# Optimization experiments

Hardware: AMD Instinct MI355X
Metric: run time of the kernel (lower is better)

The kernel has to match this reference:

```python
import jax, jax.numpy as jnp
import numpy as np

D_MODEL, D_QKV, N_HEADS, D_FFN = 2048, 128, 16, 8192
B, L = 2, 2048
EPS = 1e-8
ROPE_THETA = 10000.0


def _rope_cos_sin(seq_len, dim, dtype):
    # interleaved RoPE (rotary_embedding_torch default): pairs (0,1),(2,3),...
    inv_freq = ROPE_THETA ** (-jnp.arange(0, dim, 2, dtype=jnp.float32) / dim)
    ang = jnp.arange(seq_len, dtype=jnp.float32)[:, None] * inv_freq[None, :]  # [L, dim/2]
    return jnp.cos(ang).astype(dtype), jnp.sin(ang).astype(dtype)


def _apply_rope(t, cos, sin):
    # t: [b, h, l, d]; cos/sin: [l, d/2]
    t1, t2 = t[..., 0::2], t[..., 1::2]
    r1 = t1 * cos - t2 * sin
    r2 = t1 * sin + t2 * cos
    return jnp.stack([r1, r2], axis=-1).reshape(t.shape)


def setup_inputs() -> dict:
    key = jax.random.key(0)
    ks = jax.random.split(key, 5)
    d_out = D_QKV * N_HEADS * 3 + D_FFN * 2  # 22528
    return {
        "x": jax.random.normal(ks[0], (B, L, D_MODEL), dtype=jnp.float32),
        "g": jnp.ones((D_MODEL,), dtype=jnp.float32),
        "W_dense": jax.random.normal(ks[1], (d_out, D_MODEL), dtype=jnp.float32) * 0.02,
        "b_dense": jnp.zeros((d_out,), dtype=jnp.float32),
        "W_attn_out": jax.random.normal(ks[2], (D_MODEL, D_QKV * N_HEADS), dtype=jnp.float32) * 0.02,
        "W_ffn_out": jax.random.normal(ks[3], (D_MODEL, D_FFN), dtype=jnp.float32) * 0.02,
    }


def reference(x, g, W_dense, b_dense, W_attn_out, W_ffn_out):
    # RMSNorm (torch.norm variant): x / clamp(||x|| * d^-0.5, eps) * g
    norm = jnp.sqrt(jnp.sum(x * x, axis=-1, keepdims=True)) * (D_MODEL ** -0.5)
    normed = x / jnp.maximum(norm, EPS) * g

    h = jnp.einsum('bld,od->blo', normed, W_dense) + b_dense  # [B, L, 22528]
    dh = D_QKV * N_HEADS
    q, k, v, a, b_gate = jnp.split(h, [dh, 2 * dh, 3 * dh, 3 * dh + D_FFN], axis=-1)

    def to_heads(t):
        return t.reshape(B, L, N_HEADS, D_QKV).transpose(0, 2, 1, 3)  # [b,h,l,d]

    q, k, v = to_heads(q), to_heads(k), to_heads(v)
    cos, sin = _rope_cos_sin(L, D_QKV, x.dtype)
    q = _apply_rope(q, cos, sin)
    k = _apply_rope(k, cos, sin)

    scale = 1.0 / jnp.sqrt(jnp.asarray(D_QKV, dtype=x.dtype))
    scores = jnp.einsum('bhqd,bhkd->bhqk', q, k) * scale
    causal = jnp.tril(jnp.ones((L, L), dtype=bool))
    scores = jnp.where(causal, scores, jnp.asarray(-jnp.inf, dtype=scores.dtype))
    probs = jax.nn.softmax(scores, axis=-1)
    attn = jnp.einsum('bhqk,bhkd->bqhd', probs, v).reshape(B, L, dh)

    attn_out = jnp.einsum('blk,ok->blo', attn, W_attn_out)
    ffn_out = jnp.einsum('blf,of->blo', a * jax.nn.silu(b_gate), W_ffn_out)
    return x + attn_out + ffn_out
```

## Files before the change

kernel.cpp:

```cpp
#include <hip/hip_runtime.h>
#include <hip/hip_bf16.h>
#include <cmath>

typedef __bf16 bf16;
typedef __attribute__((ext_vector_type(8))) __bf16 bf16x8;
typedef __attribute__((ext_vector_type(4))) float f32x4;
typedef unsigned int u32;
typedef unsigned short u16;

#define D_MODEL 2048
#define NH 16
#define DQ 128
#define DH 2048
#define DFFN 8192
#define DOUT 22528
#define HQKV 6144
#define BATCH 2
#define SEQ 2048
#define NROWS 4096

__device__ __forceinline__ void gload16(const void* g, void* l) {
    __builtin_amdgcn_global_load_lds((__attribute__((address_space(1))) const void*)g,
                                     (__attribute__((address_space(3))) void*)l, 16, 0, 0);
}

__device__ __forceinline__ float bf2f(u16 u) {
    union { u32 i; float f; } c; c.i = ((u32)u) << 16; return c.f;
}

#define VMW(n)  asm volatile("s_waitcnt vmcnt(" #n ")" ::: "memory")
#define LGK0()  asm volatile("s_waitcnt lgkmcnt(0)" ::: "memory")
#define BARX()  { asm volatile("" ::: "memory"); __builtin_amdgcn_s_barrier(); asm volatile("" ::: "memory"); }

__global__ __launch_bounds__(256) void cvt_f32_bf16(const float* __restrict__ in,
                                                    bf16* __restrict__ out) {
    size_t i = ((size_t)blockIdx.x * 256 + threadIdx.x) * 8;
    float4 a = *(const float4*)(in + i);
    float4 b = *(const float4*)(in + i + 4);
    bf16x8 o;
    o[0]=(bf16)a.x; o[1]=(bf16)a.y; o[2]=(bf16)a.z; o[3]=(bf16)a.w;
    o[4]=(bf16)b.x; o[5]=(bf16)b.y; o[6]=(bf16)b.z; o[7]=(bf16)b.w;
    *(bf16x8*)(out + i) = o;
}

__global__ __launch_bounds__(256) void cvt_wd(const float* __restrict__ in,
                                              bf16* __restrict__ out) {
    size_t i = ((size_t)blockIdx.x * 256 + threadIdx.x) * 8;
    int nr = (int)(i >> 11);
    int c  = (int)(i & 2047);
    int orig;
    if (nr < HQKV) orig = nr;
    else {
        int gg = nr - HQKV;
        int blk = gg >> 4;
        int f = ((blk >> 1) << 4) + (gg & 15);
        orig = (blk & 1) ? (3*DH + DFFN + f) : (3*DH + f);
    }
    const float* src = in + (size_t)orig * 2048 + c;
    float4 a = *(const float4*)src;
    float4 b = *(const float4*)(src + 4);
    bf16x8 o;
    o[0]=(bf16)a.x; o[1]=(bf16)a.y; o[2]=(bf16)a.z; o[3]=(bf16)a.w;
    o[4]=(bf16)b.x; o[5]=(bf16)b.y; o[6]=(bf16)b.z; o[7]=(bf16)b.w;
    *(bf16x8*)(out + i) = o;
}

__global__ __launch_bounds__(256) void rmsnorm_k(const float* __restrict__ x,
                                                 const float* __restrict__ g,
                                                 bf16* __restrict__ out) {
    __shared__ float red[4];
    const int row = blockIdx.x;
    const int t = threadIdx.x;
    const float* xr = x + (size_t)row * D_MODEL;
    float4 v0 = *(const float4*)(xr + t*8);
    float4 v1 = *(const float4*)(xr + t*8 + 4);
    float ss = v0.x*v0.x + v0.y*v0.y + v0.z*v0.z + v0.w*v0.w
             + v1.x*v1.x + v1.y*v1.y + v1.z*v1.z + v1.w*v1.w;
    #pragma unroll
    for (int m = 32; m >= 1; m >>= 1) ss += __shfl_xor(ss, m);
    if ((t & 63) == 0) red[t >> 6] = ss;
    __syncthreads();
    float tot = red[0] + red[1] + red[2] + red[3];
    float norm = sqrtf(tot) * 0.022097086912079608f;
    float inv = 1.0f / fmaxf(norm, 1e-8f);
    float4 g0 = *(const float4*)(g + t*8);
    float4 g1 = *(const float4*)(g + t*8 + 4);
    bf16x8 o;
    o[0]=(bf16)(v0.x*inv*g0.x); o[1]=(bf16)(v0.y*inv*g0.y);
    o[2]=(bf16)(v0.z*inv*g0.z); o[3]=(bf16)(v0.w*inv*g0.w);
    o[4]=(bf16)(v1.x*inv*g1.x); o[5]=(bf16)(v1.y*inv*g1.y);
    o[6]=(bf16)(v1.z*inv*g1.z); o[7]=(bf16)(v1.w*inv*g1.w);
    *(bf16x8*)(out + (size_t)row * D_MODEL + t*8) = o;
}

#define SLINE_A(c_, t_) \
    gload16(Asrc + (size_t)((c_)*64)*2048 + (size_t)(t_)*64, \
            smem + (((t_)&1)<<16) + (c_)*8192 + wid*1024);
#define SLINE_B(c_, t_) \
    gload16(Bsrc + (size_t)((c_)*64)*2048 + (size_t)(t_)*64, \
            smem + (((t_)&1)<<16) + 32768 + (c_)*8192 + wid*1024);

#define PH_READS_B() \
    _Pragma("unroll") for (int n = 0; n < 4; ++n) { \
        const char* p_ = bb + (wn*64 + n*16 + la) * 128; \
        bfr[n][0] = *(const bf16x8*)(p_ + pg0); \
        bfr[n][1] = *(const bf16x8*)(p_ + pg1); }

#define PH_READS_A(qd_) \
    _Pragma("unroll") for (int mm = 0; mm < 2; ++mm) { \
        const char* p_ = ab + (wm*128 + ((qd_)*2 + mm)*16 + la) * 128; \
        af[mm][0] = *(const bf16x8*)(p_ + pg0); \
        af[mm][1] = *(const bf16x8*)(p_ + pg1); }

#define PH_MFMA(qd_) \
    __builtin_amdgcn_s_setprio(1); \
    _Pragma("unroll") for (int mm = 0; mm < 2; ++mm) \
        _Pragma("unroll") for (int n = 0; n < 4; ++n) { \
            acc[(qd_)*2+mm][n] = __builtin_amdgcn_mfma_f32_16x16x32_bf16(af[mm][0], bfr[n][0], acc[(qd_)*2+mm][n], 0, 0, 0); \
            acc[(qd_)*2+mm][n] = __builtin_amdgcn_mfma_f32_16x16x32_bf16(af[mm][1], bfr[n][1], acc[(qd_)*2+mm][n], 0, 0, 0); } \
    __builtin_amdgcn_s_setprio(0);

__global__ __launch_bounds__(512, 2) void gemm_dense(
    const bf16* __restrict__ A, const bf16* __restrict__ B,
    const float* __restrict__ bias, bf16* __restrict__ h6,
    bf16* __restrict__ ag)
{
    __shared__ char smem[131072];
    const int tid = threadIdx.x;
    const int wid = tid >> 6, lane = tid & 63;
    const int la = lane & 15, hi = lane >> 4;
    const int wm = wid >> 2, wn = wid & 3;

    const int nwg = gridDim.x;
    const int cpx = nwg >> 3;
    const int bI = blockIdx.x;
    const int wg = (bI & 7) * cpx + (bI >> 3);
    const int bn = wg >> 4, bm = wg & 15;
    const size_t m0 = (size_t)bm * 256, n0 = (size_t)bn * 256;

    const int lr = lane >> 3, lg = lane & 7;
    const int sg = lg ^ lr;
    const bf16* Asrc = A + (m0 + wid*8 + lr) * (size_t)2048 + sg*8;
    const bf16* Bsrc = B + (n0 + wid*8 + lr) * (size_t)2048 + sg*8;

    const int pg0 = (hi ^ (la & 7)) << 4;
    const int pg1 = ((4 + hi) ^ (la & 7)) << 4;

    f32x4 acc[8][4] = {};
    const int NT = 32;

    SLINE_A(0,0); SLINE_A(2,0);
    SLINE_B(0,0); SLINE_B(1,0);
    SLINE_B(2,0); SLINE_B(3,0);
    SLINE_A(1,0); SLINE_A(3,0);
    VMW(2);
    BARX();

    bf16x8 bfr[4][2];
    bf16x8 af[2][2];

    #pragma unroll 1
    for (int t = 0; t < NT - 1; ++t) {
        const char* ab = smem + ((t & 1) << 16);
        const char* bb = ab + 32768;
        const int nx = t + 1;
        PH_READS_B(); PH_READS_A(0);
        SLINE_A(0,nx); SLINE_A(2,nx);
        BARX(); LGK0(); PH_MFMA(0); BARX();
        PH_READS_A(1);
        SLINE_B(0,nx); SLINE_B(1,nx);
        BARX(); LGK0(); PH_MFMA(1); VMW(4); BARX();
        PH_READS_A(2);
        SLINE_B(2,nx); SLINE_B(3,nx);
        BARX(); LGK0(); PH_MFMA(2); BARX();
        PH_READS_A(3);
        SLINE_A(1,nx); SLINE_A(3,nx);
        BARX(); LGK0(); PH_MFMA(3); VMW(2); BARX();
    }
    {
        const int t = NT - 1;
        const char* ab = smem + ((t & 1) << 16);
        const char* bb = ab + 32768;
        PH_READS_B(); PH_READS_A(0);
        BARX(); LGK0(); PH_MFMA(0); BARX();
        PH_READS_A(1);
        BARX(); LGK0(); PH_MFMA(1); VMW(0); BARX();
        PH_READS_A(2);
        BARX(); LGK0(); PH_MFMA(2); BARX();
        PH_READS_A(3);
        BARX(); LGK0(); PH_MFMA(3); BARX();
    }

    if (n0 < HQKV) {
        #pragma unroll
        for (int mf = 0; mf < 8; ++mf) {
            const size_t row = m0 + wm*128 + mf*16 + hi*4;
            #pragma unroll
            for (int nf = 0; nf < 4; ++nf) {
                const size_t col = n0 + wn*64 + nf*16 + la;
                const float bv = bias[col];
                #pragma unroll
                for (int r = 0; r < 4; ++r)
                    h6[(row + r) * HQKV + col] = (bf16)(acc[mf][nf][r] + bv);
            }
        }
    } else {
        #pragma unroll
        for (int mf = 0; mf < 8; ++mf) {
            const size_t row = m0 + wm*128 + mf*16 + hi*4;
            #pragma unroll
            for (int np = 0; np < 4; np += 2) {
                const int col_a = (int)n0 + wn*64 + np*16 + la;
                const int gg = col_a - HQKV;
                const int f = ((gg >> 5) << 4) + (gg & 15);
                const float ba = bias[3*DH + f];
                const float bb2 = bias[3*DH + DFFN + f];
                #pragma unroll
                for (int r = 0; r < 4; ++r) {
                    float a = acc[mf][np][r] + ba;
                    float b = acc[mf][np+1][r] + bb2;
                    float sil = b / (1.0f + __expf(-b));
                    ag[(row + r) * (size_t)DFFN + f] = (bf16)(a * sil);
                }
            }
        }
    }
}

#define OSTAGE_A(st_, c_) { \
    const bf16* s_ = (st_) < 32 ? A1s + (size_t)((c_)*64)*2048 + (size_t)(st_)*64 \
                                : A2s + (size_t)((c_)*64)*8192 + (size_t)((st_)-32)*64; \
    gload16(s_, smem + ((st_)%3)*49152 + (c_)*8192 + wid*1024); }
#define OSTAGE_B(st_, c_) { \
    const bf16* s_ = (st_) < 32 ? B1s + (size_t)((c_)*64)*2048 + (size_t)(st_)*64 \
                                : B2s + (size_t)((c_)*64)*8192 + (size_t)((st_)-32)*64; \
    gload16(s_, smem + ((st_)%3)*49152 + 16384 + (c_)*8192 + wid*1024); }

__global__ __launch_bounds__(512, 2) void gemm_out(
    const bf16* __restrict__ A1, const bf16* __restrict__ B1,
    const bf16* __restrict__ A2, const bf16* __restrict__ B2,
    const float* __restrict__ x, float* __restrict__ outf)
{
    __shared__ char smem[147456];
    const int tid = threadIdx.x;
    const int wid = tid >> 6, lane = tid & 63;
    const int la = lane & 15, hi = lane >> 4;
    const int wm = wid >> 2, wn = wid & 3;

    const int nwg = gridDim.x;
    const int cpx = nwg >> 3;
    const int bI = blockIdx.x;
    const int wg = (bI & 7) * cpx + (bI >> 3);
    const int bm = wg >> 3, bn = wg & 7;
    const size_t m0 = (size_t)bm * 128, n0 = (size_t)bn * 256;

    const int lr = lane >> 3, lg = lane & 7;
    const int sg = lg ^ lr;
    const bf16* A1s = A1 + (m0 + wid*8 + lr) * (size_t)2048 + sg*8;
    const bf16* A2s = A2 + (m0 + wid*8 + lr) * (size_t)8192 + sg*8;
    const bf16* B1s = B1 + (n0 + wid*8 + lr) * (size_t)2048 + sg*8;
    const bf16* B2s = B2 + (n0 + wid*8 + lr) * (size_t)8192 + sg*8;

    const int pg0 = (hi ^ (la & 7)) << 4;
    const int pg1 = ((4 + hi) ^ (la & 7)) << 4;

    f32x4 acc[4][4] = {};
    const int NT = 160;

    OSTAGE_A(0,0); OSTAGE_A(0,1);
    OSTAGE_B(0,0); OSTAGE_B(0,1); OSTAGE_B(0,2); OSTAGE_B(0,3);
    OSTAGE_A(1,0); OSTAGE_A(1,1);
    OSTAGE_B(1,0); OSTAGE_B(1,1); OSTAGE_B(1,2); OSTAGE_B(1,3);
    VMW(6);
    BARX();

    bf16x8 af[4], bfr[4];
    #pragma unroll 1
    for (int t = 0; t < NT; ++t) {
        const char* ab = smem + (t % 3) * 49152;
        const char* bb = ab + 16384;
        const int st = t + 2;
        #pragma unroll
        for (int m = 0; m < 4; ++m) af[m]  = *(const bf16x8*)(ab + (wm*64 + m*16 + la)*128 + pg0);
        #pragma unroll
        for (int n = 0; n < 4; ++n) bfr[n] = *(const bf16x8*)(bb + (wn*64 + n*16 + la)*128 + pg0);
        if (st < NT) { OSTAGE_A(st,0); OSTAGE_A(st,1); OSTAGE_B(st,0); }
        BARX(); LGK0();
        __builtin_amdgcn_s_setprio(1);
        #pragma unroll
        for (int m = 0; m < 4; ++m)
            #pragma unroll
            for (int n = 0; n < 4; ++n)
                acc[m][n] = __builtin_amdgcn_mfma_f32_16x16x32_bf16(af[m], bfr[n], acc[m][n], 0, 0, 0);
        __builtin_amdgcn_s_setprio(0);
        BARX();
        #pragma unroll
        for (int m = 0; m < 4; ++m) af[m]  = *(const bf16x8*)(ab + (wm*64 + m*16 + la)*128 + pg1);
        #pragma unroll
        for (int n = 0; n < 4; ++n) bfr[n] = *(const bf16x8*)(bb + (wn*64 + n*16 + la)*128 + pg1);
        if (st < NT) { OSTAGE_B(st,1); OSTAGE_B(st,2); OSTAGE_B(st,3); }
        if (t < NT - 2) { VMW(6); } else { VMW(0); }
        BARX(); LGK0();
        __builtin_amdgcn_s_setprio(1);
        #pragma unroll
        for (int m = 0; m < 4; ++m)
            #pragma unroll
            for (int n = 0; n < 4; ++n)
                acc[m][n] = __builtin_amdgcn_mfma_f32_16x16x32_bf16(af[m], bfr[n], acc[m][n], 0, 0, 0);
        __builtin_amdgcn_s_setprio(0);
        BARX();
    }

    #pragma unroll
    for (int mf = 0; mf < 4; ++mf) {
        const size_t row = m0 + wm*64 + mf*16 + hi*4;
        #pragma unroll
        for (int nf = 0; nf < 4; ++nf) {
            const size_t col = n0 + wn*64 + nf*16 + la;
            #pragma unroll
            for (int r = 0; r < 4; ++r) {
                const size_t off = (row + r) * (size_t)DH + col;
                outf[off] = x[off] + acc[mf][nf][r];
            }
        }
    }
}

__global__ __launch_bounds__(256) void rope_table(float* __restrict__ ctab,
                                                  float* __restrict__ stab) {
    int idx = blockIdx.x * 256 + threadIdx.x;
    int l = idx >> 6, i = idx & 63;
    float inv = powf(10000.0f, -(float)i / 64.0f);
    float ang = (float)l * inv;
    float s, c;
    sincosf(ang, &s, &c);
    ctab[idx] = c; stab[idx] = s;
}

__device__ __forceinline__ u32 rope_pair(u32 u, float c, float s) {
    float t1 = bf2f((u16)(u & 0xffff));
    float t2 = bf2f((u16)(u >> 16));
    float r1 = t1 * c - t2 * s;
    float r2 = t1 * s + t2 * c;
    bf16 b1 = (bf16)r1, b2 = (bf16)r2;
    return (u32)__builtin_bit_cast(u16, b1) | ((u32)__builtin_bit_cast(u16, b2) << 16);
}

__global__ __launch_bounds__(256) void rope_qk(const bf16* __restrict__ h,
                                               const float* __restrict__ ctab,
                                               const float* __restrict__ stab,
                                               bf16* __restrict__ qb, bf16* __restrict__ kb) {
    int idx = blockIdx.x * 256 + threadIdx.x;
    int i  = idx & 63;
    int hh = (idx >> 6) & 15;
    int l  = (idx >> 10) & 2047;
    int b  = idx >> 21;
    size_t hrow = (size_t)(b * SEQ + l) * HQKV;
    float c = ctab[l*64 + i], s = stab[l*64 + i];
    u32 uq = *(const u32*)(h + hrow + hh*DQ + 2*i);
    u32 uk = *(const u32*)(h + hrow + DH + hh*DQ + 2*i);
    size_t orow = ((size_t)(b*NH + hh) * SEQ + l) * DQ + 2*i;
    *(u32*)(qb + orow) = rope_pair(uq, c, s);
    *(u32*)(kb + orow) = rope_pair(uk, c, s);
}

__global__ __launch_bounds__(256) void v_transpose(const bf16* __restrict__ h,
                                                   bf16* __restrict__ vt) {
    __shared__ u32 lds[64][68];
    const int lt = blockIdx.x, bh = blockIdx.y;
    const int b = bh >> 4, hh = bh & 15;
    const int t = threadIdx.x;
    const bf16* src = h + (size_t)(b * SEQ + lt * 64) * HQKV + 2*DH + hh * DQ;
    #pragma unroll
    for (int i = 0; i < 4; ++i) {
        int j = i*256 + t;
        int l = j >> 4, ch = j & 15;
        uint4 v = *(const uint4*)(src + (size_t)l * HQKV + ch*8);
        *(uint4*)&lds[l][ch*4] = v;
    }
    __syncthreads();
    bf16* dst = vt + (size_t)bh * DQ * SEQ + lt * 64;
    #pragma unroll
    for (int i = 0; i < 4; ++i) {
        int j = i*256 + t;
        int d = j >> 3, lc = j & 7;
        u32 out[4];
        #pragma unroll
        for (int m = 0; m < 4; ++m) {
            u32 a0 = lds[lc*8 + 2*m][d >> 1];
            u32 a1 = lds[lc*8 + 2*m + 1][d >> 1];
            u16 s0 = (d & 1) ? (u16)(a0 >> 16) : (u16)(a0 & 0xffff);
            u16 s1 = (d & 1) ? (u16)(a1 >> 16) : (u16)(a1 & 0xffff);
            out[m] = (u32)s0 | ((u32)s1 << 16);
        }
        *(uint4*)(dst + (size_t)d * SEQ + lc*8) = *(uint4*)out;
    }
}

__global__ __launch_bounds__(256) void attn_fa(const bf16* __restrict__ Q,
                                               const bf16* __restrict__ Kb,
                                               const bf16* __restrict__ Vt,
                                               bf16* __restrict__ O) {
    __shared__ bf16 Ks[64][128];
    __shared__ bf16 Vts[128][64];
    __shared__ bf16 Ps[4][16][64];
    const int qt = blockIdx.x, bh = blockIdx.y;
    const int b = bh >> 4, hh = bh & 15;
    const int tid = threadIdx.x, wid = tid >> 6, lane = tid & 63;
    const int la = lane & 15, hi = lane >> 4;
    const bf16* Qp = Q + (size_t)bh * SEQ * DQ;
    const bf16* Kp = Kb + (size_t)bh * SEQ * DQ;
    const bf16* Vp = Vt + (size_t)bh * DQ * SEQ;
    const int q0w = qt * 64 + wid * 16;

    bf16x8 qf[4];
    #pragma unroll
    for (int s = 0; s < 4; ++s)
        qf[s] = *(const bf16x8*)(Qp + (size_t)(q0w + la) * DQ + s*32 + hi*8);

    f32x4 acc_o[8] = {};
    float m_run[4] = {-1e30f, -1e30f, -1e30f, -1e30f};
    float l_run[4] = {0.f, 0.f, 0.f, 0.f};
    const float scale = 0.08838834764831845f;

    const int nk = qt + 1;
    for (int kt = 0; kt < nk; ++kt) {
        const int k0 = kt * 64;
        __syncthreads();
        #pragma unroll
        for (int i = 0; i < 4; ++i) {
            int j = i*256 + tid;
            int kr = j >> 4, jg = j & 15;
            gload16(Kp + (size_t)(k0 + kr) * DQ + ((jg ^ (kr & 7)) << 3),
                    (char*)Ks + i*4096 + wid*1024);
            int d = j >> 3, vg = j & 7;
            gload16(Vp + (size_t)d * SEQ + k0 + ((vg ^ (d & 7)) << 3),
                    (char*)Vts + i*4096 + wid*1024);
        }
        __syncthreads();

        f32x4 sacc[4] = {};
        __builtin_amdgcn_s_setprio(1);
        #pragma unroll
        for (int g = 0; g < 4; ++g) {
            const int krow = g*16 + la;
            #pragma unroll
            for (int s = 0; s < 4; ++s) {
                bf16x8 kf = *(const bf16x8*)((const char*)Ks + krow*256 + (((s*4 + hi) ^ (la & 7)) << 4));
                sacc[g] = __builtin_amdgcn_mfma_f32_16x16x32_bf16(qf[s], kf, sacc[g], 0, 0, 0);
            }
        }
        __builtin_amdgcn_s_setprio(0);

        float mnew[4];
        #pragma unroll
        for (int r = 0; r < 4; ++r) mnew[r] = m_run[r];
        #pragma unroll
        for (int g = 0; g < 4; ++g)
            #pragma unroll
            for (int r = 0; r < 4; ++r) {
                float sv = sacc[g][r] * scale;
                int qi = q0w + hi*4 + r;
                int ki = k0 + g*16 + la;
                sv = (ki <= qi) ? sv : -1e30f;
                sacc[g][r] = sv;
                mnew[r] = fmaxf(mnew[r], sv);
            }
        #pragma unroll
        for (int r = 0; r < 4; ++r) {
            float v = mnew[r];
            v = fmaxf(v, __shfl_xor(v, 1));
            v = fmaxf(v, __shfl_xor(v, 2));
            v = fmaxf(v, __shfl_xor(v, 4));
            v = fmaxf(v, __shfl_xor(v, 8));
            mnew[r] = v;
        }
        float resc[4], lsum[4];
        #pragma unroll
        for (int r = 0; r < 4; ++r) {
            resc[r] = __expf(m_run[r] - mnew[r]);
            m_run[r] = mnew[r];
            lsum[r] = 0.f;
        }
        #pragma unroll
        for (int g = 0; g < 4; ++g)
            #pragma unroll
            for (int r = 0; r < 4; ++r) {
                float p = __expf(sacc[g][r] - mnew[r]);
                sacc[g][r] = p;
                lsum[r] += p;
            }
        #pragma unroll
        for (int r = 0; r < 4; ++r) {
            float v = lsum[r];
            v += __shfl_xor(v, 1); v += __shfl_xor(v, 2);
            v += __shfl_xor(v, 4); v += __shfl_xor(v, 8);
            l_run[r] = l_run[r] * resc[r] + v;
        }
        #pragma unroll
        for (int g = 0; g < 4; ++g)
            #pragma unroll
            for (int r = 0; r < 4; ++r) {
                int prow = hi*4 + r;
                int pcol = (g*16 + la) ^ ((prow & 7) << 3);
                Ps[wid][prow][pcol] = (bf16)sacc[g][r];
            }
        #pragma unroll
        for (int n = 0; n < 8; ++n)
            #pragma unroll
            for (int r = 0; r < 4; ++r) acc_o[n][r] *= resc[r];
        __builtin_amdgcn_s_setprio(1);
        #pragma unroll
        for (int kk = 0; kk < 2; ++kk) {
            bf16x8 pf = *(const bf16x8*)((const char*)&Ps[wid][0][0] + la*128 +
                                         (((kk*32 + hi*8) ^ ((la & 7) << 3)) << 1));
            #pragma unroll
            for (int n = 0; n < 8; ++n) {
                const int vrow = n*16 + la;
                bf16x8 vf = *(const bf16x8*)((const char*)Vts + vrow*128 + (((kk*4 + hi) ^ (la & 7)) << 4));
                acc_o[n] = __builtin_amdgcn_mfma_f32_16x16x32_bf16(pf, vf, acc_o[n], 0, 0, 0);
            }
        }
        __builtin_amdgcn_s_setprio(0);
    }

    bf16* Op = O + (size_t)b * SEQ * DH + (size_t)hh * DQ;
    #pragma unroll
    for (int r = 0; r < 4; ++r) {
        int qi = q0w + hi*4 + r;
        float invl = 1.0f / l_run[r];
        #pragma unroll
        for (int n = 0; n < 8; ++n)
            Op[(size_t)qi * DH + n*16 + la] = (bf16)(acc_o[n][r] * invl);
    }
}

extern "C" void kernel_launch(void* const* d_in, const int* in_sizes, int n_in,
                              void* d_out, int out_size, void* d_ws, size_t ws_size,
                              hipStream_t stream) {
    const float* x       = (const float*)d_in[0];
    const float* g       = (const float*)d_in[1];
    const float* W_dense = (const float*)d_in[2];
    const float* b_dense = (const float*)d_in[3];
    const float* W_attn  = (const float*)d_in[4];
    const float* W_ffn   = (const float*)d_in[5];
    float* out = (float*)d_out;

    char* ws = (char*)d_ws;
    bf16* normed  = (bf16*)(ws + 0);
    bf16* Wd_b    = (bf16*)(ws + 16777216);
    bf16* Wa_b    = (bf16*)(ws + 109051904);
    bf16* Wf_b    = (bf16*)(ws + 117440512);
    bf16* h_b     = (bf16*)(ws + 150994944);
    bf16* ag_b    = (bf16*)(ws + 335544320);
    float* ctab   = (float*)(ws + 402653184);
    float* stab   = (float*)(ws + 403177472);
    bf16* q_b  = (bf16*)(ws + 16777216);
    bf16* k_b  = (bf16*)(ws + 16777216 + 16777216);
    bf16* vt_b = (bf16*)(ws + 16777216 + 33554432);
    bf16* attn_b = normed;

    cvt_wd<<<46137344/2048, 256, 0, stream>>>(W_dense, Wd_b);
    cvt_f32_bf16<<<4194304/2048, 256, 0, stream>>>(W_attn, Wa_b);
    cvt_f32_bf16<<<16777216/2048, 256, 0, stream>>>(W_ffn, Wf_b);
    rmsnorm_k<<<NROWS, 256, 0, stream>>>(x, g, normed);
    {
        dim3 grid((NROWS/256) * (DOUT/256));
        gemm_dense<<<grid, 512, 0, stream>>>(normed, Wd_b, b_dense, h_b, ag_b);
    }
    rope_table<<<SEQ*64/256, 256, 0, stream>>>(ctab, stab);
    rope_qk<<<4194304/256, 256, 0, stream>>>(h_b, ctab, stab, q_b, k_b);
    {
        dim3 grid(SEQ/64, BATCH*NH);
        v_transpose<<<grid, 256, 0, stream>>>(h_b, vt_b);
    }
    {
        dim3 grid(SEQ/64, BATCH*NH);
        attn_fa<<<grid, 256, 0, stream>>>(q_b, k_b, vt_b, attn_b);
    }
    gemm_out<<<256, 512, 0, stream>>>(attn_b, Wa_b, ag_b, Wf_b, x, out);
}
```

Baseline: 819.9 us.

## Deepen GEMM LDS pipeline to five slots and double-buffer attention K/V

```diff
diff --git a/kernel.cpp b/kernel.cpp
--- a/kernel.cpp
+++ b/kernel.cpp
@@ -93,12 +93,12 @@
     *(bf16x8*)(out + (size_t)row * D_MODEL + t*8) = o;
 }
 
-#define SLINE_A(c_, t_) \
-    gload16(Asrc + (size_t)((c_)*64)*2048 + (size_t)(t_)*64, \
-            smem + (((t_)&1)<<16) + (c_)*8192 + wid*1024);
-#define SLINE_B(c_, t_) \
-    gload16(Bsrc + (size_t)((c_)*64)*2048 + (size_t)(t_)*64, \
-            smem + (((t_)&1)<<16) + 32768 + (c_)*8192 + wid*1024);
+#define SL_A(c_, tt_) \
+    gload16(Asrc + (size_t)((c_)*64)*2048 + (size_t)(tt_)*64, \
+            smem + ((2*(tt_))%5)*32768 + (c_)*8192 + wid*1024);
+#define SL_B(c_, tt_) \
+    gload16(Bsrc + (size_t)((c_)*64)*2048 + (size_t)(tt_)*64, \
+            smem + ((2*(tt_)+1)%5)*32768 + (c_)*8192 + wid*1024);
 
 #define PH_READS_B() \
     _Pragma("unroll") for (int n = 0; n < 4; ++n) { \
@@ -125,7 +125,7 @@
     const float* __restrict__ bias, bf16* __restrict__ h6,
     bf16* __restrict__ ag)
 {
-    __shared__ char smem[131072];
+    __shared__ char smem[163840];
     const int tid = threadIdx.x;
     const int wid = tid >> 6, lane = tid & 63;
     const int la = lane & 15, hi = lane >> 4;
@@ -149,45 +149,32 @@
     f32x4 acc[8][4] = {};
     const int NT = 32;
 
-    SLINE_A(0,0); SLINE_A(2,0);
-    SLINE_B(0,0); SLINE_B(1,0);
-    SLINE_B(2,0); SLINE_B(3,0);
-    SLINE_A(1,0); SLINE_A(3,0);
-    VMW(2);
+    SL_A(0,0); SL_A(1,0); SL_A(2,0); SL_A(3,0);
+    SL_B(0,0); SL_B(1,0); SL_B(2,0); SL_B(3,0);
+    SL_A(0,1); SL_A(1,1); SL_A(2,1); SL_A(3,1);
+    VMW(4);
     BARX();
 
     bf16x8 bfr[4][2];
     bf16x8 af[2][2];
 
     #pragma unroll 1
-    for (int t = 0; t < NT - 1; ++t) {
-        const char* ab = smem + ((t & 1) << 16);
-        const char* bb = ab + 32768;
-        const int nx = t + 1;
+    for (int t = 0; t < NT; ++t) {
+        const char* ab = smem + ((2*t)%5)*32768;
+        const char* bb = smem + ((2*t+1)%5)*32768;
         PH_READS_B(); PH_READS_A(0);
-        SLINE_A(0,nx); SLINE_A(2,nx);
+        if (t+1 < NT) { SL_B(0,t+1); SL_B(1,t+1); }
         BARX(); LGK0(); PH_MFMA(0); BARX();
         PH_READS_A(1);
-        SLINE_B(0,nx); SLINE_B(1,nx);
-        BARX(); LGK0(); PH_MFMA(1); VMW(4); BARX();
+        if (t+1 < NT) { SL_B(2,t+1); SL_B(3,t+1); }
+        BARX(); LGK0(); PH_MFMA(1); BARX();
         PH_READS_A(2);
-        SLINE_B(2,nx); SLINE_B(3,nx);
+        if (t+2 < NT) { SL_A(0,t+2); SL_A(2,t+2); }
         BARX(); LGK0(); PH_MFMA(2); BARX();
         PH_READS_A(3);
-        SLINE_A(1,nx); SLINE_A(3,nx);
-        BARX(); LGK0(); PH_MFMA(3); VMW(2); BARX();
-    }
-    {
-        const int t = NT - 1;
-        const char* ab = smem + ((t & 1) << 16);
-        const char* bb = ab + 32768;
-        PH_READS_B(); PH_READS_A(0);
-        BARX(); LGK0(); PH_MFMA(0); BARX();
-        PH_READS_A(1);
-        BARX(); LGK0(); PH_MFMA(1); VMW(0); BARX();
-        PH_READS_A(2);
-        BARX(); LGK0(); PH_MFMA(2); BARX();
-        PH_READS_A(3);
+        if (t+2 < NT) { SL_A(1,t+2); SL_A(3,t+2); }
+        if (t+2 < NT)      { VMW(4); }
+        else if (t+1 < NT) { VMW(0); }
         BARX(); LGK0(); PH_MFMA(3); BARX();
     }
 
@@ -401,8 +388,7 @@
                                                const bf16* __restrict__ Kb,
                                                const bf16* __restrict__ Vt,
                                                bf16* __restrict__ O) {
-    __shared__ bf16 Ks[64][128];
-    __shared__ bf16 Vts[128][64];
+    __shared__ char kvs[2][32768];
     __shared__ bf16 Ps[4][16][64];
     const int qt = blockIdx.x, bh = blockIdx.y;
     const int b = bh >> 4, hh = bh & 15;
@@ -422,22 +408,28 @@
     float m_run[4] = {-1e30f, -1e30f, -1e30f, -1e30f};
     float l_run[4] = {0.f, 0.f, 0.f, 0.f};
     const float scale = 0.08838834764831845f;
-
     const int nk = qt + 1;
+
+#define ATT_STAGE(kt_, buf_) { \
+    const int k0_ = (kt_) * 64; \
+    _Pragma("unroll") for (int i = 0; i < 4; ++i) { \
+        int j = i*256 + tid; \
+        int kr = j >> 4, jg = j & 15; \
+        gload16(Kp + (size_t)(k0_ + kr) * DQ + ((jg ^ (kr & 7)) << 3), \
+                kvs[buf_] + i*4096 + wid*1024); \
+        int d = j >> 3, vg = j & 7; \
+        gload16(Vp + (size_t)d * SEQ + k0_ + ((vg ^ (d & 7)) << 3), \
+                kvs[buf_] + 16384 + i*4096 + wid*1024); \
+    } }
+
+    ATT_STAGE(0, 0);
+
     for (int kt = 0; kt < nk; ++kt) {
         const int k0 = kt * 64;
-        __syncthreads();
-        #pragma unroll
-        for (int i = 0; i < 4; ++i) {
-            int j = i*256 + tid;
-            int kr = j >> 4, jg = j & 15;
-            gload16(Kp + (size_t)(k0 + kr) * DQ + ((jg ^ (kr & 7)) << 3),
-                    (char*)Ks + i*4096 + wid*1024);
-            int d = j >> 3, vg = j & 7;
-            gload16(Vp + (size_t)d * SEQ + k0 + ((vg ^ (d & 7)) << 3),
-                    (char*)Vts + i*4096 + wid*1024);
-        }
-        __syncthreads();
+        const char* kb2 = kvs[kt & 1];
+        if (kt + 1 < nk) { ATT_STAGE(kt+1, (kt+1)&1); VMW(8); }
+        else             { VMW(0); }
+        BARX();
 
         f32x4 sacc[4] = {};
         __builtin_amdgcn_s_setprio(1);
@@ -446,7 +438,7 @@
             const int krow = g*16 + la;
             #pragma unroll
             for (int s = 0; s < 4; ++s) {
-                bf16x8 kf = *(const bf16x8*)((const char*)Ks + krow*256 + (((s*4 + hi) ^ (la & 7)) << 4));
+                bf16x8 kf = *(const bf16x8*)(kb2 + krow*256 + (((s*4 + hi) ^ (la & 7)) << 4));
                 sacc[g] = __builtin_amdgcn_mfma_f32_16x16x32_bf16(qf[s], kf, sacc[g], 0, 0, 0);
             }
         }
@@ -517,11 +509,12 @@
             #pragma unroll
             for (int n = 0; n < 8; ++n) {
                 const int vrow = n*16 + la;
-                bf16x8 vf = *(const bf16x8*)((const char*)Vts + vrow*128 + (((kk*4 + hi) ^ (la & 7)) << 4));
+                bf16x8 vf = *(const bf16x8*)(kb2 + 16384 + vrow*128 + (((kk*4 + hi) ^ (la & 7)) << 4));
                 acc_o[n] = __builtin_amdgcn_mfma_f32_16x16x32_bf16(pf, vf, acc_o[n], 0, 0, 0);
             }
         }
         __builtin_amdgcn_s_setprio(0);
+        BARX();
     }
 
     bf16* Op = O + (size_t)b * SEQ * DH + (size_t)hh * DQ;
```

Measured after the change: 821.1 us. About the same (+0.1%).

## Fuse RoPE into dense GEMM epilogue and double-buffer K/V loads in attention

Applied to the files above, without the earlier changes.

```diff
diff --git a/kernel.cpp b/kernel.cpp
--- a/kernel.cpp
+++ b/kernel.cpp
@@ -93,6 +93,17 @@
     *(bf16x8*)(out + (size_t)row * D_MODEL + t*8) = o;
 }
 
+__global__ __launch_bounds__(256) void rope_table(float* __restrict__ ctab,
+                                                  float* __restrict__ stab) {
+    int idx = blockIdx.x * 256 + threadIdx.x;
+    int l = idx >> 6, i = idx & 63;
+    float inv = powf(10000.0f, -(float)i / 64.0f);
+    float ang = (float)l * inv;
+    float s, c;
+    sincosf(ang, &s, &c);
+    ctab[idx] = c; stab[idx] = s;
+}
+
 #define SLINE_A(c_, t_) \
     gload16(Asrc + (size_t)((c_)*64)*2048 + (size_t)(t_)*64, \
             smem + (((t_)&1)<<16) + (c_)*8192 + wid*1024);
@@ -122,8 +133,10 @@
 
 __global__ __launch_bounds__(512, 2) void gemm_dense(
     const bf16* __restrict__ A, const bf16* __restrict__ B,
-    const float* __restrict__ bias, bf16* __restrict__ h6,
-    bf16* __restrict__ ag)
+    const float* __restrict__ bias,
+    const float* __restrict__ ctab, const float* __restrict__ stab,
+    bf16* __restrict__ qb, bf16* __restrict__ kb,
+    bf16* __restrict__ vbuf, bf16* __restrict__ ag)
 {
     __shared__ char smem[131072];
     const int tid = threadIdx.x;
@@ -191,17 +204,42 @@
         BARX(); LGK0(); PH_MFMA(3); BARX();
     }
 
-    if (n0 < HQKV) {
+    if (n0 < 2*DH) {
+        bf16* dst = (n0 < DH) ? qb : kb;
+        #pragma unroll
+        for (int mf = 0; mf < 8; ++mf) {
+            const int row = (int)m0 + wm*128 + mf*16 + hi*4;
+            #pragma unroll
+            for (int nf = 0; nf < 4; ++nf) {
+                const int col = (int)n0 + wn*64 + nf*16 + la;
+                const int dcol = col & 127;
+                const int hh = (col >> 7) & 15;
+                const int ii = dcol >> 1;
+                const float bv = bias[col];
+                #pragma unroll
+                for (int r = 0; r < 4; ++r) {
+                    const int rw = row + r;
+                    const int l = rw & 2047, bidx = rw >> 11;
+                    float v = acc[mf][nf][r] + bv;
+                    float pv = __shfl_xor(v, 1);
+                    const float c = ctab[l*64 + ii];
+                    const float s = stab[l*64 + ii];
+                    float o = (la & 1) ? (pv * s + v * c) : (v * c - pv * s);
+                    dst[(((size_t)(bidx*NH + hh)) * SEQ + l) * DQ + dcol] = (bf16)o;
+                }
+            }
+        }
+    } else if (n0 < 3*DH) {
         #pragma unroll
         for (int mf = 0; mf < 8; ++mf) {
             const size_t row = m0 + wm*128 + mf*16 + hi*4;
             #pragma unroll
             for (int nf = 0; nf < 4; ++nf) {
-                const size_t col = n0 + wn*64 + nf*16 + la;
+                const int col = (int)n0 + wn*64 + nf*16 + la;
                 const float bv = bias[col];
                 #pragma unroll
                 for (int r = 0; r < 4; ++r)
-                    h6[(row + r) * HQKV + col] = (bf16)(acc[mf][nf][r] + bv);
+                    vbuf[(row + r) * (size_t)DH + (col - 2*DH)] = (bf16)(acc[mf][nf][r] + bv);
             }
         }
     } else {
@@ -326,56 +364,18 @@
     }
 }
 
-__global__ __launch_bounds__(256) void rope_table(float* __restrict__ ctab,
-                                                  float* __restrict__ stab) {
-    int idx = blockIdx.x * 256 + threadIdx.x;
-    int l = idx >> 6, i = idx & 63;
-    float inv = powf(10000.0f, -(float)i / 64.0f);
-    float ang = (float)l * inv;
-    float s, c;
-    sincosf(ang, &s, &c);
-    ctab[idx] = c; stab[idx] = s;
-}
-
-__device__ __forceinline__ u32 rope_pair(u32 u, float c, float s) {
-    float t1 = bf2f((u16)(u & 0xffff));
-    float t2 = bf2f((u16)(u >> 16));
-    float r1 = t1 * c - t2 * s;
-    float r2 = t1 * s + t2 * c;
-    bf16 b1 = (bf16)r1, b2 = (bf16)r2;
-    return (u32)__builtin_bit_cast(u16, b1) | ((u32)__builtin_bit_cast(u16, b2) << 16);
-}
-
-__global__ __launch_bounds__(256) void rope_qk(const bf16* __restrict__ h,
-                                               const float* __restrict__ ctab,
-                                               const float* __restrict__ stab,
-                                               bf16* __restrict__ qb, bf16* __restrict__ kb) {
-    int idx = blockIdx.x * 256 + threadIdx.x;
-    int i  = idx & 63;
-    int hh = (idx >> 6) & 15;
-    int l  = (idx >> 10) & 2047;
-    int b  = idx >> 21;
-    size_t hrow = (size_t)(b * SEQ + l) * HQKV;
-    float c = ctab[l*64 + i], s = stab[l*64 + i];
-    u32 uq = *(const u32*)(h + hrow + hh*DQ + 2*i);
-    u32 uk = *(const u32*)(h + hrow + DH + hh*DQ + 2*i);
-    size_t orow = ((size_t)(b*NH + hh) * SEQ + l) * DQ + 2*i;
-    *(u32*)(qb + orow) = rope_pair(uq, c, s);
-    *(u32*)(kb + orow) = rope_pair(uk, c, s);
-}
-
-__global__ __launch_bounds__(256) void v_transpose(const bf16* __restrict__ h,
+__global__ __launch_bounds__(256) void v_transpose(const bf16* __restrict__ vbuf,
                                                    bf16* __restrict__ vt) {
     __shared__ u32 lds[64][68];
     const int lt = blockIdx.x, bh = blockIdx.y;
     const int b = bh >> 4, hh = bh & 15;
     const int t = threadIdx.x;
-    const bf16* src = h + (size_t)(b * SEQ + lt * 64) * HQKV + 2*DH + hh * DQ;
+    const bf16* src = vbuf + (size_t)(b * SEQ + lt * 64) * DH + hh * DQ;
     #pragma unroll
     for (int i = 0; i < 4; ++i) {
         int j = i*256 + t;
         int l = j >> 4, ch = j & 15;
-        uint4 v = *(const uint4*)(src + (size_t)l * HQKV + ch*8);
+        uint4 v = *(const uint4*)(src + (size_t)l * DH + ch*8);
         *(uint4*)&lds[l][ch*4] = v;
     }
     __syncthreads();
@@ -401,8 +401,7 @@
                                                const bf16* __restrict__ Kb,
                                                const bf16* __restrict__ Vt,
                                                bf16* __restrict__ O) {
-    __shared__ bf16 Ks[64][128];
-    __shared__ bf16 Vts[128][64];
+    __shared__ char kvs[2][32768];
     __shared__ bf16 Ps[4][16][64];
     const int qt = blockIdx.x, bh = blockIdx.y;
     const int b = bh >> 4, hh = bh & 15;
@@ -422,22 +421,28 @@
     float m_run[4] = {-1e30f, -1e30f, -1e30f, -1e30f};
     float l_run[4] = {0.f, 0.f, 0.f, 0.f};
     const float scale = 0.08838834764831845f;
-
     const int nk = qt + 1;
+
+#define ATT_STAGE(kt_, buf_) { \
+    const int k0_ = (kt_) * 64; \
+    _Pragma("unroll") for (int i = 0; i < 4; ++i) { \
+        int j = i*256 + tid; \
+        int kr = j >> 4, jg = j & 15; \
+        gload16(Kp + (size_t)(k0_ + kr) * DQ + ((jg ^ (kr & 7)) << 3), \
+                kvs[buf_] + i*4096 + wid*1024); \
+        int d = j >> 3, vg = j & 7; \
+        gload16(Vp + (size_t)d * SEQ + k0_ + ((vg ^ (d & 7)) << 3), \
+                kvs[buf_] + 16384 + i*4096 + wid*1024); \
+    } }
+
+    ATT_STAGE(0, 0);
+
     for (int kt = 0; kt < nk; ++kt) {
         const int k0 = kt * 64;
-        __syncthreads();
-        #pragma unroll
-        for (int i = 0; i < 4; ++i) {
-            int j = i*256 + tid;
-            int kr = j >> 4, jg = j & 15;
-            gload16(Kp + (size_t)(k0 + kr) * DQ + ((jg ^ (kr & 7)) << 3),
-                    (char*)Ks + i*4096 + wid*1024);
-            int d = j >> 3, vg = j & 7;
-            gload16(Vp + (size_t)d * SEQ + k0 + ((vg ^ (d & 7)) << 3),
-                    (char*)Vts + i*4096 + wid*1024);
-        }
-        __syncthreads();
+        const char* kb2 = kvs[kt & 1];
+        if (kt + 1 < nk) { ATT_STAGE(kt+1, (kt+1)&1); VMW(8); }
+        else             { VMW(0); }
+        BARX();
 
         f32x4 sacc[4] = {};
         __builtin_amdgcn_s_setprio(1);
@@ -446,7 +451,7 @@
             const int krow = g*16 + la;
             #pragma unroll
             for (int s = 0; s < 4; ++s) {
-                bf16x8 kf = *(const bf16x8*)((const char*)Ks + krow*256 + (((s*4 + hi) ^ (la & 7)) << 4));
+                bf16x8 kf = *(const bf16x8*)(kb2 + krow*256 + (((s*4 + hi) ^ (la & 7)) << 4));
                 sacc[g] = __builtin_amdgcn_mfma_f32_16x16x32_bf16(qf[s], kf, sacc[g], 0, 0, 0);
             }
         }
@@ -517,11 +522,12 @@
             #pragma unroll
             for (int n = 0; n < 8; ++n) {
                 const int vrow = n*16 + la;
-                bf16x8 vf = *(const bf16x8*)((const char*)Vts + vrow*128 + (((kk*4 + hi) ^ (la & 7)) << 4));
+                bf16x8 vf = *(const bf16x8*)(kb2 + 16384 + vrow*128 + (((kk*4 + hi) ^ (la & 7)) << 4));
                 acc_o[n] = __builtin_amdgcn_mfma_f32_16x16x32_bf16(pf, vf, acc_o[n], 0, 0, 0);
             }
         }
         __builtin_amdgcn_s_setprio(0);
+        BARX();
     }
 
     bf16* Op = O + (size_t)b * SEQ * DH + (size_t)hh * DQ;
@@ -551,28 +557,28 @@
     bf16* Wd_b    = (bf16*)(ws + 16777216);
     bf16* Wa_b    = (bf16*)(ws + 109051904);
     bf16* Wf_b    = (bf16*)(ws + 117440512);
-    bf16* h_b     = (bf16*)(ws + 150994944);
+    bf16* q_b     = (bf16*)(ws + 150994944);
+    bf16* k_b     = (bf16*)(ws + 167772160);
+    bf16* vbuf    = (bf16*)(ws + 184549376);
+    bf16* vt_b    = (bf16*)(ws + 201326592);
     bf16* ag_b    = (bf16*)(ws + 335544320);
     float* ctab   = (float*)(ws + 402653184);
     float* stab   = (float*)(ws + 403177472);
-    bf16* q_b  = (bf16*)(ws + 16777216);
-    bf16* k_b  = (bf16*)(ws + 16777216 + 16777216);
-    bf16* vt_b = (bf16*)(ws + 16777216 + 33554432);
-    bf16* attn_b = normed;
+    bf16* attn_b  = normed;
 
     cvt_wd<<<46137344/2048, 256, 0, stream>>>(W_dense, Wd_b);
     cvt_f32_bf16<<<4194304/2048, 256, 0, stream>>>(W_attn, Wa_b);
     cvt_f32_bf16<<<16777216/2048, 256, 0, stream>>>(W_ffn, Wf_b);
     rmsnorm_k<<<NROWS, 256, 0, stream>>>(x, g, normed);
+    rope_table<<<SEQ*64/256, 256, 0, stream>>>(ctab, stab);
     {
         dim3 grid((NROWS/256) * (DOUT/256));
-        gemm_dense<<<grid, 512, 0, stream>>>(normed, Wd_b, b_dense, h_b, ag_b);
-    }
-    rope_table<<<SEQ*64/256, 256, 0, stream>>>(ctab, stab);
-    rope_qk<<<4194304/256, 256, 0, stream>>>(h_b, ctab, stab, q_b, k_b);
+        gemm_dense<<<grid, 512, 0, stream>>>(normed, Wd_b, b_dense, ctab, stab,
+                                             q_b, k_b, vbuf, ag_b);
+    }
     {
         dim3 grid(SEQ/64, BATCH*NH);
-        v_transpose<<<grid, 256, 0, stream>>>(h_b, vt_b);
+        v_transpose<<<grid, 256, 0, stream>>>(vbuf, vt_b);
     }
     {
         dim3 grid(SEQ/64, BATCH*NH);
```

Measured after the change: 827.7 us. About the same (+0.9%).

## Double-buffer K/V tiles in flash attention and remap gemm_out tile order

Applied to the files above, without the earlier changes.

```diff
diff --git a/kernel.cpp b/kernel.cpp
--- a/kernel.cpp
+++ b/kernel.cpp
@@ -93,6 +93,17 @@
     *(bf16x8*)(out + (size_t)row * D_MODEL + t*8) = o;
 }
 
+__global__ __launch_bounds__(256) void rope_table(float* __restrict__ ctab,
+                                                  float* __restrict__ stab) {
+    int idx = blockIdx.x * 256 + threadIdx.x;
+    int l = idx >> 6, i = idx & 63;
+    float inv = powf(10000.0f, -(float)i / 64.0f);
+    float ang = (float)l * inv;
+    float s, c;
+    sincosf(ang, &s, &c);
+    ctab[idx] = c; stab[idx] = s;
+}
+
 #define SLINE_A(c_, t_) \
     gload16(Asrc + (size_t)((c_)*64)*2048 + (size_t)(t_)*64, \
             smem + (((t_)&1)<<16) + (c_)*8192 + wid*1024);
@@ -251,7 +262,7 @@
     const int cpx = nwg >> 3;
     const int bI = blockIdx.x;
     const int wg = (bI & 7) * cpx + (bI >> 3);
-    const int bm = wg >> 3, bn = wg & 7;
+    const int bm = wg & 31, bn = wg >> 5;
     const size_t m0 = (size_t)bm * 128, n0 = (size_t)bn * 256;
 
     const int lr = lane >> 3, lg = lane & 7;
@@ -311,6 +322,8 @@
         BARX();
     }
 
+    const int wmL = wid >> 2, wnL = wid & 3;
+    (void)wmL; (void)wnL;
     #pragma unroll
     for (int mf = 0; mf < 4; ++mf) {
         const size_t row = m0 + wm*64 + mf*16 + hi*4;
@@ -324,17 +337,6 @@
             }
         }
     }
-}
-
-__global__ __launch_bounds__(256) void rope_table(float* __restrict__ ctab,
-                                                  float* __restrict__ stab) {
-    int idx = blockIdx.x * 256 + threadIdx.x;
-    int l = idx >> 6, i = idx & 63;
-    float inv = powf(10000.0f, -(float)i / 64.0f);
-    float ang = (float)l * inv;
-    float s, c;
-    sincosf(ang, &s, &c);
-    ctab[idx] = c; stab[idx] = s;
 }
 
 __device__ __forceinline__ u32 rope_pair(u32 u, float c, float s) {
@@ -401,8 +403,7 @@
                                                const bf16* __restrict__ Kb,
                                                const bf16* __restrict__ Vt,
                                                bf16* __restrict__ O) {
-    __shared__ bf16 Ks[64][128];
-    __shared__ bf16 Vts[128][64];
+    __shared__ char kvs[2][32768];
     __shared__ bf16 Ps[4][16][64];
     const int qt = blockIdx.x, bh = blockIdx.y;
     const int b = bh >> 4, hh = bh & 15;
@@ -422,22 +423,28 @@
     float m_run[4] = {-1e30f, -1e30f, -1e30f, -1e30f};
     float l_run[4] = {0.f, 0.f, 0.f, 0.f};
     const float scale = 0.08838834764831845f;
-
     const int nk = qt + 1;
+
+#define ATT_STAGE(kt_, buf_) { \
+    const int k0_ = (kt_) * 64; \
+    _Pragma("unroll") for (int i = 0; i < 4; ++i) { \
+        int j = i*256 + tid; \
+        int kr = j >> 4, jg = j & 15; \
+        gload16(Kp + (size_t)(k0_ + kr) * DQ + ((jg ^ (kr & 7)) << 3), \
+                kvs[buf_] + i*4096 + wid*1024); \
+        int d = j >> 3, vg = j & 7; \
+        gload16(Vp + (size_t)d * SEQ + k0_ + ((vg ^ (d & 7)) << 3), \
+                kvs[buf_] + 16384 + i*4096 + wid*1024); \
+    } }
+
+    ATT_STAGE(0, 0);
+
     for (int kt = 0; kt < nk; ++kt) {
         const int k0 = kt * 64;
-        __syncthreads();
-        #pragma unroll
-        for (int i = 0; i < 4; ++i) {
-            int j = i*256 + tid;
-            int kr = j >> 4, jg = j & 15;
-            gload16(Kp + (size_t)(k0 + kr) * DQ + ((jg ^ (kr & 7)) << 3),
-                    (char*)Ks + i*4096 + wid*1024);
-            int d = j >> 3, vg = j & 7;
-            gload16(Vp + (size_t)d * SEQ + k0 + ((vg ^ (d & 7)) << 3),
-                    (char*)Vts + i*4096 + wid*1024);
-        }
-        __syncthreads();
+        const char* kb2 = kvs[kt & 1];
+        if (kt + 1 < nk) { ATT_STAGE(kt+1, (kt+1)&1); VMW(8); }
+        else             { VMW(0); }
+        BARX();
 
         f32x4 sacc[4] = {};
         __builtin_amdgcn_s_setprio(1);
@@ -446,7 +453,7 @@
             const int krow = g*16 + la;
             #pragma unroll
             for (int s = 0; s < 4; ++s) {
-                bf16x8 kf = *(const bf16x8*)((const char*)Ks + krow*256 + (((s*4 + hi) ^ (la & 7)) << 4));
+                bf16x8 kf = *(const bf16x8*)(kb2 + krow*256 + (((s*4 + hi) ^ (la & 7)) << 4));
                 sacc[g] = __builtin_amdgcn_mfma_f32_16x16x32_bf16(qf[s], kf, sacc[g], 0, 0, 0);
             }
         }
@@ -517,11 +524,12 @@
             #pragma unroll
             for (int n = 0; n < 8; ++n) {
                 const int vrow = n*16 + la;
-                bf16x8 vf = *(const bf16x8*)((const char*)Vts + vrow*128 + (((kk*4 + hi) ^ (la & 7)) << 4));
+                bf16x8 vf = *(const bf16x8*)(kb2 + 16384 + vrow*128 + (((kk*4 + hi) ^ (la & 7)) << 4));
                 acc_o[n] = __builtin_amdgcn_mfma_f32_16x16x32_bf16(pf, vf, acc_o[n], 0, 0, 0);
             }
         }
         __builtin_amdgcn_s_setprio(0);
+        BARX();
     }
 
     bf16* Op = O + (size_t)b * SEQ * DH + (size_t)hh * DQ;
@@ -564,11 +572,11 @@
     cvt_f32_bf16<<<4194304/2048, 256, 0, stream>>>(W_attn, Wa_b);
     cvt_f32_bf16<<<16777216/2048, 256, 0, stream>>>(W_ffn, Wf_b);
     rmsnorm_k<<<NROWS, 256, 0, stream>>>(x, g, normed);
+    rope_table<<<SEQ*64/256, 256, 0, stream>>>(ctab, stab);
     {
         dim3 grid((NROWS/256) * (DOUT/256));
         gemm_dense<<<grid, 512, 0, stream>>>(normed, Wd_b, b_dense, h_b, ag_b);
     }
-    rope_table<<<SEQ*64/256, 256, 0, stream>>>(ctab, stab);
     rope_qk<<<4194304/256, 256, 0, stream>>>(h_b, ctab, stab, q_b, k_b);
     {
         dim3 grid(SEQ/64, BATCH*NH);
```

New measurement: 822.6 us. No clear change (+0.3%).
